# Kernel optimization log

Hardware: AMD Instinct MI355X
Metric: run time of the kernel (lower is better)

## Reference

```python
import jax, jax.numpy as jnp
import numpy as np

E, C, L, B = 8, 128, 1024, 32
FB = L // 2 + 1        # 513 freq bins
HD = 2 * FB            # 1026 hidden dim


def setup_inputs() -> dict:
    key = jax.random.key(0)
    ks = jax.random.split(key, 8)
    return {
        "X_time": jax.random.normal(ks[0], (B, C, L), jnp.float32),
        "bound_params": jax.random.normal(ks[1], (E - 1,), jnp.float32),
        "W1r": jax.random.normal(ks[2], (E, HD, FB), jnp.float32) * 0.1,
        "W1i": jax.random.normal(ks[3], (E, HD, FB), jnp.float32) * 0.1,
        "b1r": jnp.zeros((E, HD), jnp.float32),
        "b1i": jnp.zeros((E, HD), jnp.float32),
        "W2r": jax.random.normal(ks[4], (E, FB, HD), jnp.float32) * 0.1,
        "W2i": jax.random.normal(ks[5], (E, FB, HD), jnp.float32) * 0.1,
        "b2r": jnp.zeros((E, FB), jnp.float32),
        "b2i": jnp.zeros((E, FB), jnp.float32),
        "gate_W": jax.random.normal(ks[6], (E, FB), jnp.float32) * 0.1,
        "gate_b": jnp.zeros((E,), jnp.float32),
    }


def reference(X_time, bound_params, W1r, W1i, b1r, b1i, W2r, W2i, b2r, b2i, gate_W, gate_b):
    Bx, Cx, Lx = X_time.shape
    fb = Lx // 2 + 1
    e = W1r.shape[0]

    Xf = jnp.fft.rfft(X_time, axis=-1)                     # [B,C,FB] complex

    # learnable frequency-band binary masks
    raw = jax.nn.sigmoid(bound_params)
    bounds = jnp.sort(jnp.concatenate([jnp.zeros(1, raw.dtype), raw, jnp.ones(1, raw.dtype)]))
    idx = (bounds * (fb - 1)).astype(jnp.int32)
    starts = idx[:e]
    ends = jnp.concatenate([idx[1:e], jnp.array([fb], jnp.int32)])
    pos = jnp.arange(fb)
    masks = ((pos[None, :] >= starts[:, None]) & (pos[None, :] < ends[:, None])).astype(X_time.dtype)  # [E,FB]

    # masked spectra per expert, split into real/imag: [E,B,C,FB]
    m = masks[:, None, None, :]
    xr = Xf.real * m
    xi = Xf.imag * m

    # expert layer 1: complex linear (W [E,HD,FB]) + complex ReLU
    hr = jnp.einsum('ehf,ebcf->ebch', W1r, xr) - jnp.einsum('ehf,ebcf->ebch', W1i, xi) + b1r[:, None, None, :]
    hi = jnp.einsum('ehf,ebcf->ebch', W1r, xi) + jnp.einsum('ehf,ebcf->ebch', W1i, xr) + b1i[:, None, None, :]
    hr = jax.nn.relu(hr)
    hi = jax.nn.relu(hi)

    # expert layer 2: complex linear (W [E,FB,HD]) -> [E,B,C,FB]
    yr = jnp.einsum('efh,ebch->ebcf', W2r, hr) - jnp.einsum('efh,ebch->ebcf', W2i, hi) + b2r[:, None, None, :]
    yi = jnp.einsum('efh,ebch->ebcf', W2r, hi) + jnp.einsum('efh,ebch->ebcf', W2i, hr) + b2i[:, None, None, :]

    # gate: mean |Xf| over channels -> linear -> softmax over experts
    mag = jnp.mean(jnp.abs(Xf), axis=1)                    # [B,FB]
    gate = jax.nn.softmax(mag @ gate_W.T + gate_b, axis=-1)  # [B,E]

    comb_r = jnp.einsum('ebcf,be->bcf', yr, gate)
    comb_i = jnp.einsum('ebcf,be->bcf', yi, gate)
    return jnp.fft.irfft(jax.lax.complex(comb_r, comb_i), n=Lx, axis=-1)
```

## Files before the change

### kernel.cpp

```cpp
#include <hip/hip_runtime.h>
#include <hip/hip_bf16.h>
#include <math.h>

typedef __hip_bfloat16 bf16;
typedef __attribute__((ext_vector_type(8))) short short8;
typedef __attribute__((ext_vector_type(4))) float f32x4;

#define FB 513
#define HD 1026
#define NN 1024
#define MR 4096
#define NE 8
#define BATCH 32

#define XINT_LD 1280
#define BIAS_LD 1056
#define FINV_LD 1088
#define HP_LD   2080
#define B1_ROWS 2176
#define KCAT    16640
#define MAG_LD  520
#define FF_ROWS 1280

__device__ __forceinline__ void gload16(const void* g, void* l) {
    __builtin_amdgcn_global_load_lds((const __attribute__((address_space(1))) void*)g,
                                     (__attribute__((address_space(3))) void*)l, 16, 0, 0);
}
__device__ __forceinline__ bf16 f2b(float v) { return __float2bfloat16(v); }
__device__ __forceinline__ unsigned short f2bu(float v) {
    bf16 b = __float2bfloat16(v);
    return *reinterpret_cast<unsigned short*>(&b);
}
__device__ __forceinline__ float bu2f(unsigned short u) {
    return __uint_as_float(((unsigned)u) << 16);
}
__device__ __forceinline__ unsigned pack2(float a, float b) {
    return (unsigned)f2bu(a) | ((unsigned)f2bu(b) << 16);
}

__device__ __forceinline__ void xcd_swizzle(int* px, int* py) {
    int gx = gridDim.x;
    int orig = blockIdx.x + gx * blockIdx.y;
    int q = (gx * gridDim.y) >> 3;
    int wg = (orig & 7) * q + (orig >> 3);
    *px = wg % gx;
    *py = wg / gx;
}

__global__ void prep_kernel(const float* __restrict__ bp, int* __restrict__ se) {
    if (threadIdx.x == 0 && blockIdx.x == 0) {
        float b[9];
        b[0] = 0.0f; b[8] = 1.0f;
        for (int i = 0; i < 7; i++) b[i + 1] = 1.0f / (1.0f + expf(-bp[i]));
        for (int i = 1; i < 9; i++) { float v = b[i]; int j = i - 1;
            while (j >= 0 && b[j] > v) { b[j + 1] = b[j]; j--; } b[j + 1] = v; }
        int idx[9];
        for (int i = 0; i < 9; i++) idx[i] = (int)(b[i] * (float)(FB - 1));
        for (int e = 0; e < NE; e++) {
            se[2 * e] = idx[e];
            se[2 * e + 1] = (e < NE - 1) ? idx[e + 1] : FB;
        }
    }
}

#define N_FF  ((long)FF_ROWS * NN)
#define N_FI  (1024L * FINV_LD)
#define N_B1P ((long)NE * B1_ROWS * (XINT_LD / 2))
#define N_XP  ((long)MR * NN / 2)
#define N_PREP (N_FF + N_FI + N_B1P + N_XP)

__global__ void prep_bulk(const float* __restrict__ W1r, const float* __restrict__ W1i,
                          const float* __restrict__ X, const int* __restrict__ se,
                          bf16* __restrict__ Ffwd, bf16* __restrict__ Finv,
                          bf16* __restrict__ B1, bf16* __restrict__ Xb) {
    long i = (long)blockIdx.x * 256 + threadIdx.x;
    const float TWO_PI = 6.283185307179586f;
    if (i < N_FF) {
        int n = (int)(i >> 10), t = (int)(i & (NN - 1));
        float v = 0.0f;
        if (n < 2 * FB) {
            int f = n >> 1, k = (f * t) & (NN - 1);
            float s, c; sincosf(TWO_PI * (float)k / (float)NN, &s, &c);
            v = (n & 1) ? -s : c;
        }
        Ffwd[i] = f2b(v);
        return;
    }
    i -= N_FF;
    if (i < N_FI) {
        int t = (int)(i / FINV_LD), k = (int)(i % FINV_LD);
        float v = 0.0f;
        if (k < 2 * FB) {
            int f = k >> 1, kk = (f * t) & (NN - 1);
            float s, c; sincosf(TWO_PI * (float)kk / (float)NN, &s, &c);
            float cf = (f == 0 || f == FB - 1) ? 1.0f : 2.0f;
            float sc = cf * (1.0f / (float)NN);
            v = (k & 1) ? -s * sc : c * sc;
        }
        Finv[i] = f2b(v);
        return;
    }
    i -= N_FI;
    if (i < N_B1P) {
        int f = (int)(i % (XINT_LD / 2));
        long t = i / (XINT_LD / 2);
        int n = (int)(t % B1_ROWS);
        int e = (int)(t / B1_ROWS);
        float ve = 0.0f, vo = 0.0f;
        if (n < 2 * HD && f < FB && f >= se[2 * e] && f < se[2 * e + 1]) {
            int hi_part = (n >= HD);
            int h = hi_part ? n - HD : n;
            long wi = ((long)e * HD + h) * FB + f;
            float wr = W1r[wi], wim = W1i[wi];
            ve = hi_part ? wim : wr;
            vo = hi_part ? wr : -wim;
        }
        *(unsigned*)(B1 + ((size_t)(e * B1_ROWS + n)) * XINT_LD + 2 * f) = pack2(ve, vo);
        return;
    }
    i -= N_B1P;
    if (i < N_XP) {
        float2 v = ((const float2*)X)[i];
        *(unsigned*)(Xb + 2 * i) = pack2(v.x, v.y);
    }
}

__global__ void pack_B2t(const float* __restrict__ W2r, const float* __restrict__ W2i,
                         bf16* __restrict__ B2t) {
    __shared__ float sR[64][65], sI[64][65];
    int e = blockIdx.z;
    int f0 = blockIdx.x * 64;
    int h0 = blockIdx.y * 64;
    int tid = threadIdx.x;
#pragma unroll
    for (int rep = 0; rep < 16; rep++) {
        int idx = tid + rep * 256;
        int fl = idx >> 6, hl = idx & 63;
        int f = f0 + fl, h = h0 + hl;
        bool ok = (f < FB) && (h < HD);
        size_t wi = ((size_t)e * FB + f) * HD + h;
        sR[fl][hl] = ok ? W2r[wi] : 0.0f;
        sI[fl][hl] = ok ? W2i[wi] : 0.0f;
    }
    __syncthreads();
#pragma unroll
    for (int rep = 0; rep < 4; rep++) {
        int idx = tid + rep * 256;
        int hl = idx >> 4, ch = idx & 15;
        int h = h0 + hl;
        int c0 = 2 * f0 + ch * 8;
        if (c0 >= FINV_LD) continue;
        short8 lo, hi;
#pragma unroll
        for (int j = 0; j < 4; j++) {
            int fl = ch * 4 + j;
            float wr = sR[fl][hl], wim = sI[fl][hl];
            lo[2 * j]     = (short)f2bu(wr);
            lo[2 * j + 1] = (short)f2bu(wim);
            hi[2 * j]     = (short)f2bu(-wim);
            hi[2 * j + 1] = (short)f2bu(wr);
        }
        if (h < HD) {
            *(short8*)(B2t + ((size_t)e * HP_LD + h) * FINV_LD + c0) = lo;
            *(short8*)(B2t + ((size_t)e * HP_LD + HD + h) * FINV_LD + c0) = hi;
        } else if (HD + h < HP_LD) {
            short8 z = {};
            *(short8*)(B2t + ((size_t)e * HP_LD + HD + h) * FINV_LD + c0) = z;
        }
    }
}

__global__ void mag_kernel(const bf16* __restrict__ Xint, float* __restrict__ magp) {
    int b = blockIdx.x, g = blockIdx.y, t = threadIdx.x;
    float acc[3] = {0.0f, 0.0f, 0.0f};
    const bf16* base = Xint + ((size_t)b * 128 + g * 16) * XINT_LD;
    for (int c = 0; c < 16; c++) {
        const bf16* row = base + (size_t)c * XINT_LD;
#pragma unroll
        for (int kk = 0; kk < 3; kk++) {
            int f = t + 256 * kk;
            if (f < FB) {
                float xr = __bfloat162float(row[2 * f]);
                float xi = __bfloat162float(row[2 * f + 1]);
                acc[kk] += sqrtf(xr * xr + xi * xi);
            }
        }
    }
#pragma unroll
    for (int kk = 0; kk < 3; kk++) {
        int f = t + 256 * kk;
        if (f < FB) magp[((size_t)b * 8 + g) * MAG_LD + f] = acc[kk];
    }
}

__global__ void gate_bias_kernel(const float* __restrict__ magp, const float* __restrict__ gW,
                                 const float* __restrict__ gb, const float* __restrict__ b2r,
                                 const float* __restrict__ b2i, float* __restrict__ gate,
                                 float* __restrict__ biasCs) {
    __shared__ float sred[256];
    __shared__ float sg[8];
    int b = blockIdx.x, tid = threadIdx.x;
    int e = tid & 7, j = tid >> 3;
    float acc = 0.0f;
    for (int f = j; f < FB; f += 32) {
        float m = 0.0f;
#pragma unroll
        for (int g = 0; g < 8; g++) m += magp[((size_t)b * 8 + g) * MAG_LD + f];
        acc += m * (1.0f / 128.0f) * gW[e * FB + f];
    }
    sred[tid] = acc;
    __syncthreads();
    if (tid < 64) {
        float a = sred[tid] + sred[tid + 64] + sred[tid + 128] + sred[tid + 192];
        a += __shfl_xor(a, 8); a += __shfl_xor(a, 16); a += __shfl_xor(a, 32);
        float logit = a + gb[e];
        float mx = logit;
        mx = fmaxf(mx, __shfl_xor(mx, 1)); mx = fmaxf(mx, __shfl_xor(mx, 2)); mx = fmaxf(mx, __shfl_xor(mx, 4));
        float ex = expf(logit - mx);
        float sum = ex;
        sum += __shfl_xor(sum, 1); sum += __shfl_xor(sum, 2); sum += __shfl_xor(sum, 4);
        if (tid < 8) { float g_ = ex / sum; sg[tid] = g_; gate[b * NE + tid] = g_; }
    }
    __syncthreads();
    for (int c = tid; c < BIAS_LD; c += 256) {
        float v = 0.0f;
        if (c < 2 * FB) {
            int f = c >> 1;
            const float* bb = (c & 1) ? b2i : b2r;
#pragma unroll
            for (int ee = 0; ee < NE; ee++) v += sg[ee] * bb[ee * FB + f];
            float cf = (f == 0 || f == FB - 1) ? 1.0f : 2.0f;
            v *= cf * (1.0f / (float)NN);
        }
        biasCs[b * BIAS_LD + c] = v;
    }
}

__global__ void biasT_kernel(const float* __restrict__ biasCs, const bf16* __restrict__ Ffwd,
                             float* __restrict__ biasT) {
    int t = blockIdx.x * 256 + threadIdx.x;
    int b = blockIdx.y;
    float s = 0.0f;
    for (int c = 0; c < 2 * FB; c++)
        s += biasCs[b * BIAS_LD + c] * __bfloat162float(Ffwd[(size_t)c * NN + t]);
    biasT[b * NN + t] = s;
}

__global__ void reduce_out4(const bf16* __restrict__ planes, const float* __restrict__ biasT,
                            float* __restrict__ out) {
    long idx = (long)blockIdx.x * 256 + threadIdx.x;
    if (idx >= (long)MR * NN / 8) return;
    size_t base = (size_t)idx * 8;
    long r = base >> 10;
    int t = (int)(base & (NN - 1));
    float s[8] = {};
#pragma unroll
    for (int z = 0; z < 4; z++) {
        short8 v = *(const short8*)(planes + (size_t)z * MR * NN + base);
#pragma unroll
        for (int j = 0; j < 8; j++) s[j] += bu2f((unsigned short)v[j]);
    }
    const float* bT = biasT + (r >> 7) * NN + t;
    float4 o0 = {s[0] + bT[0], s[1] + bT[1], s[2] + bT[2], s[3] + bT[3]};
    float4 o1 = {s[4] + bT[4], s[5] + bT[5], s[6] + bT[6], s[7] + bT[7]};
    *(float4*)(out + base) = o0;
    *(float4*)(out + base + 4) = o1;
}

template <int EPI>
__global__ void gemm_mfma(const bf16* __restrict__ A, int lda,
                          const bf16* __restrict__ B, int ldb, size_t zBstride,
                          void* __restrict__ Cv, int ldc, size_t zCoff,
                          int N, int K, int kPerZ,
                          const int* __restrict__ se2,
                          const float* __restrict__ biasR, const float* __restrict__ biasI,
                          int zBias, const float* __restrict__ gate8) {
    __shared__ bf16 As[128 * 32];
    __shared__ bf16 Bs[128 * 32];
    int tid = threadIdx.x;
    int zz = blockIdx.z;
    int bx, by;
    xcd_swizzle(&bx, &by);
    int row0 = by * 128, col0 = bx * 128;
    const bf16* Bz = B + (size_t)zz * zBstride;

    int kS, kE;
    if (EPI == 1) { int s = se2[2 * zz], e = se2[2 * zz + 1]; kS = (2 * s) & ~31; kE = (2 * e + 31) & ~31; }
    else          { kS = zz * kPerZ; kE = min(K, kS + kPerZ); }

    f32x4 acc[4][4] = {};

    int lane = tid & 63, wid = tid >> 6;
    int wrB = (wid >> 1) << 6, wcB = (wid & 1) << 6;
    int lr = lane & 15, lk = (lane >> 4) << 3;

    int r_a = tid >> 2, c_a = (tid & 3) << 3;
    int r_b = (tid + 256) >> 2, c_b = ((tid + 256) & 3) << 3;

    for (int kt = kS; kt < kE; kt += 32) {
        gload16(A + (size_t)(row0 + r_a) * lda + kt + c_a, &As[(size_t)tid * 8]);
        gload16(A + (size_t)(row0 + r_b) * lda + kt + c_b, &As[((size_t)tid + 256) * 8]);
        gload16(Bz + (size_t)(col0 + r_a) * ldb + kt + c_a, &Bs[(size_t)tid * 8]);
        gload16(Bz + (size_t)(col0 + r_b) * ldb + kt + c_b, &Bs[((size_t)tid + 256) * 8]);
        __syncthreads();
        short8 av[4], bv[4];
#pragma unroll
        for (int m = 0; m < 4; m++)
            av[m] = *(const short8*)&As[(wrB + m * 16 + lr) * 32 + lk];
#pragma unroll
        for (int n = 0; n < 4; n++)
            bv[n] = *(const short8*)&Bs[(wcB + n * 16 + lr) * 32 + lk];
#pragma unroll
        for (int m = 0; m < 4; m++)
#pragma unroll
            for (int n = 0; n < 4; n++)
                acc[m][n] = __builtin_amdgcn_mfma_f32_16x16x32_bf16(av[m], bv[n], acc[m][n], 0, 0, 0);
        __syncthreads();
    }

    int r0 = row0 + wrB + ((lane >> 4) << 2);
    int c0i = col0 + wcB + (lane & 15);
    float g = (EPI == 1) ? gate8[(row0 >> 7) * NE + zz] : 0.0f;

#pragma unroll
    for (int m = 0; m < 4; m++)
#pragma unroll
        for (int n = 0; n < 4; n++) {
            int c = c0i + n * 16;
            if (c >= N) continue;
#pragma unroll
            for (int j = 0; j < 4; j++) {
                int r = r0 + m * 16 + j;
                float v = acc[m][n][j];
                if (EPI == 1) {
                    v += (c < HD) ? biasR[zz * zBias + c] : biasI[zz * zBias + c - HD];
                    v = fmaxf(v, 0.0f) * g;
                    ((bf16*)Cv + (size_t)zz * zCoff)[(size_t)r * ldc + c] = f2b(v);
                } else {
                    ((float*)Cv + (size_t)zz * zCoff)[(size_t)r * ldc + c] = v;
                }
            }
        }
}

__device__ __forceinline__ void stage_half(const bf16* gbase, int ld, int kt,
                                           bf16* ldsBase, int tid) {
#pragma unroll
    for (int j = 0; j < 2; j++) {
        int r = j * 64 + (tid >> 3);
        int sc = ((tid & 7) ^ ((tid >> 3) & 7)) * 8;
        gload16(gbase + (size_t)r * ld + kt + sc, ldsBase + j * 4096 + tid * 8);
    }
}

#define MF(a, b, c) __builtin_amdgcn_mfma_f32_16x16x32_bf16(a, b, c, 0, 0, 0)
#define RD(off) (*(const short8*)(bc + (off)))

#define PHASE_MFMA(FM)                                                        \
    {                                                                         \
        short8 aa0 = RD(aBase + (FM) * 1024 + cb0);                           \
        short8 aa1 = RD(aBase + (FM) * 1024 + cb1);                           \
        short8 ab0 = RD(aBase + (FM + 1) * 1024 + cb0);                       \
        short8 ab1 = RD(aBase + (FM + 1) * 1024 + cb1);                       \
        __builtin_amdgcn_s_setprio(1);                                        \
        acc[FM][0] = MF(aa0, b0[0], acc[FM][0]);                              \
        acc[FM][0] = MF(aa1, b1[0], acc[FM][0]);                              \
        acc[FM][1] = MF(aa0, b0[1], acc[FM][1]);                              \
        acc[FM][1] = MF(aa1, b1[1], acc[FM][1]);                              \
        acc[FM][2] = MF(aa0, b0[2], acc[FM][2]);                              \
        acc[FM][2] = MF(aa1, b1[2], acc[FM][2]);                              \
        acc[FM][3] = MF(aa0, b0[3], acc[FM][3]);                              \
        acc[FM][3] = MF(aa1, b1[3], acc[FM][3]);                              \
        acc[FM + 1][0] = MF(ab0, b0[0], acc[FM + 1][0]);                      \
        acc[FM + 1][0] = MF(ab1, b1[0], acc[FM + 1][0]);                      \
        acc[FM + 1][1] = MF(ab0, b0[1], acc[FM + 1][1]);                      \
        acc[FM + 1][1] = MF(ab1, b1[1], acc[FM + 1][1]);                      \
        acc[FM + 1][2] = MF(ab0, b0[2], acc[FM + 1][2]);                      \
        acc[FM + 1][2] = MF(ab1, b1[2], acc[FM + 1][2]);                      \
        acc[FM + 1][3] = MF(ab0, b0[3], acc[FM + 1][3]);                      \
        acc[FM + 1][3] = MF(ab1, b1[3], acc[FM + 1][3]);                      \
        __builtin_amdgcn_s_setprio(0);                                        \
        __builtin_amdgcn_sched_barrier(0);                                    \
        __builtin_amdgcn_s_barrier();                                         \
    }

template <int SWZ>
__global__ __launch_bounds__(512, 2) void gemm8p(
        const bf16* __restrict__ A, int lda, const bf16* __restrict__ B, int ldb,
        bf16* __restrict__ C, int ldc, size_t zCoff,
        int tilesPerZ, int totTiles, int gx) {
    __shared__ bf16 sm[65536];
    int tid = threadIdx.x;
    int id = blockIdx.x;
    int bx, by, z;
    if (SWZ == 1) {
        int by_z = (id & 7) * 8 + (id >> 5);
        bx = (id >> 3) & 3;
        z = by_z >> 4;
        by = by_z & 15;
    } else {
        bx = id % gx; by = id / gx; z = 0;
    }
    int row0 = by * 256, col0 = bx * 256;
    int t0 = z * tilesPerZ;
    int nt = min(tilesPerZ, totTiles - t0);
    int kS = t0 * 64;

    const bf16* Ab = A + (size_t)row0 * lda;
    const bf16* Bb = B + (size_t)col0 * ldb;

    stage_half(Ab, lda, kS, sm, tid);
    stage_half(Ab + (size_t)128 * lda, lda, kS, sm + 8192, tid);
    stage_half(Bb, ldb, kS, sm + 16384, tid);
    stage_half(Bb + (size_t)128 * ldb, ldb, kS, sm + 24576, tid);

    f32x4 acc[8][4] = {};

    int l = tid & 63, w = tid >> 6;
    int wm = w >> 2, wn = w & 3;
    int lr = l & 15, lk4 = l >> 4;
    int swz = lr & 7;
    int cb0 = ((lk4) ^ swz) * 8;
    int cb1 = ((4 + lk4) ^ swz) * 8;
    int aBaseR = wm * 8192 + lr * 64;
    int bBaseR = 16384 + (wn >> 1) * 8192 + (wn & 1) * 4096 + lr * 64;

    for (int t = 0; t < nt; ++t) {
        const int cur = t & 1;
        const bf16* bc = sm + cur * 32768;
        bf16* bufN = sm + (cur ^ 1) * 32768;
        int aBase = aBaseR, bBase = bBaseR;
        int ktn = kS + (t + 1) * 64;
        bool more = (t + 1) < nt;
        if (more) {
            stage_half(Ab, lda, ktn, bufN, tid);
            stage_half(Ab + (size_t)128 * lda, lda, ktn, bufN + 8192, tid);
            asm volatile("s_waitcnt vmcnt(4)" ::: "memory");
        } else {
            asm volatile("s_waitcnt vmcnt(0)" ::: "memory");
        }
        __builtin_amdgcn_s_barrier();
        __builtin_amdgcn_sched_barrier(0);
        short8 b0[4], b1[4];
#pragma unroll
        for (int n = 0; n < 4; n++) {
            b0[n] = RD(bBase + n * 1024 + cb0);
            b1[n] = RD(bBase + n * 1024 + cb1);
        }
        PHASE_MFMA(0)
        if (more) {
            stage_half(Bb, ldb, ktn, bufN + 16384, tid);
            stage_half(Bb + (size_t)128 * ldb, ldb, ktn, bufN + 24576, tid);
        }
        PHASE_MFMA(2)
        PHASE_MFMA(4)
        PHASE_MFMA(6)
    }

    bf16* Cp = C + (size_t)z * zCoff;
    int rb = row0 + wm * 128 + lk4 * 4;
    int cbase = col0 + wn * 64 + lr;
#pragma unroll
    for (int fm = 0; fm < 8; fm++)
#pragma unroll
        for (int n = 0; n < 4; n++)
#pragma unroll
            for (int j = 0; j < 4; j++)
                Cp[(size_t)(rb + fm * 16 + j) * ldc + cbase + n * 16] = f2b(acc[fm][n][j]);
}

extern "C" void kernel_launch(void* const* d_in, const int* in_sizes, int n_in,
                              void* d_out, int out_size, void* d_ws, size_t ws_size,
                              hipStream_t stream) {
    const float* X   = (const float*)d_in[0];
    const float* bp  = (const float*)d_in[1];
    const float* W1r = (const float*)d_in[2];
    const float* W1i = (const float*)d_in[3];
    const float* b1r = (const float*)d_in[4];
    const float* b1i = (const float*)d_in[5];
    const float* W2r = (const float*)d_in[6];
    const float* W2i = (const float*)d_in[7];
    const float* b2r = (const float*)d_in[8];
    const float* b2i = (const float*)d_in[9];
    const float* gW  = (const float*)d_in[10];
    const float* gb  = (const float*)d_in[11];
    float* out = (float*)d_out;

    const size_t SZH = (size_t)MR * HP_LD * 2;

    char* p = (char*)d_ws;
    auto alloc = [&](size_t bytes) -> char* {
        char* r = p; p += (bytes + 255) & ~255ULL; return r;
    };
    int*   se     = (int*)alloc(64 * 4);
    float* magp   = (float*)alloc((size_t)BATCH * 8 * MAG_LD * 4);
    float* gate   = (float*)alloc((size_t)BATCH * NE * 4);
    float* biasCs = (float*)alloc((size_t)BATCH * BIAS_LD * 4);
    float* biasT  = (float*)alloc((size_t)BATCH * NN * 4);
    bf16*  Ffwd   = (bf16*)alloc((size_t)FF_ROWS * NN * 2);
    bf16*  Finv   = (bf16*)alloc((size_t)NN * FINV_LD * 2);
    bf16*  B1     = (bf16*)alloc((size_t)NE * B1_ROWS * XINT_LD * 2);
    bf16*  B2t    = (bf16*)alloc((size_t)KCAT * FINV_LD * 2);
    bf16*  Xint   = (bf16*)alloc((size_t)MR * XINT_LD * 2);
    bf16*  planesB = (bf16*)alloc(4 * (size_t)MR * NN * 2);
    bf16*  Hp     = (bf16*)alloc(8 * SZH);
    bf16*  B2inv  = (bf16*)B1;
    bf16*  Xb     = (bf16*)((char*)Hp + 8 * SZH - (size_t)MR * NN * 2);

    prep_kernel<<<1, 64, 0, stream>>>(bp, se);
    prep_bulk<<<(unsigned)((N_PREP + 255) / 256), 256, 0, stream>>>(
        W1r, W1i, X, se, Ffwd, Finv, B1, Xb);
    pack_B2t<<<dim3(9, 17, 8), 256, 0, stream>>>(W2r, W2i, B2t);

    gemm8p<0><<<80, 512, 0, stream>>>(
        Xb, NN, Ffwd, NN, Xint, XINT_LD, 0, 16, 16, 5);

    mag_kernel<<<dim3(BATCH, 8), 256, 0, stream>>>(Xint, magp);
    gate_bias_kernel<<<BATCH, 256, 0, stream>>>(magp, gW, gb, b2r, b2i, gate, biasCs);
    biasT_kernel<<<dim3(4, BATCH), 256, 0, stream>>>(biasCs, Ffwd, biasT);

    gemm_mfma<1><<<dim3(17, 32, 8), 256, 0, stream>>>(
        Xint, XINT_LD, B1, XINT_LD, (size_t)B1_ROWS * XINT_LD,
        Hp, KCAT, HP_LD, 2 * HD, 0, 0,
        se, b1r, b1i, HD, gate);

    gemm8p<0><<<260, 512, 0, stream>>>(
        Finv, FINV_LD, B2t, FINV_LD, B2inv, KCAT, 0, 17, 17, 65);

    gemm8p<1><<<256, 512, 0, stream>>>(
        Hp, KCAT, B2inv, KCAT, planesB, NN, (size_t)MR * NN, 65, 260, 4);

    reduce_out4<<<(unsigned)(((size_t)MR * NN / 8 + 255) / 256), 256, 0, stream>>>(
        planesB, biasT, out);
}
```

Baseline: 415.5 us.

## Fold band-bound prep into bulk kernel and prefetch A fragments ahead in gemm8p

```diff
diff --git a/kernel.cpp b/kernel.cpp
--- a/kernel.cpp
+++ b/kernel.cpp
@@ -47,20 +47,13 @@
     *py = wg / gx;
 }
 
-__global__ void prep_kernel(const float* __restrict__ bp, int* __restrict__ se) {
-    if (threadIdx.x == 0 && blockIdx.x == 0) {
-        float b[9];
-        b[0] = 0.0f; b[8] = 1.0f;
-        for (int i = 0; i < 7; i++) b[i + 1] = 1.0f / (1.0f + expf(-bp[i]));
-        for (int i = 1; i < 9; i++) { float v = b[i]; int j = i - 1;
-            while (j >= 0 && b[j] > v) { b[j + 1] = b[j]; j--; } b[j + 1] = v; }
-        int idx[9];
-        for (int i = 0; i < 9; i++) idx[i] = (int)(b[i] * (float)(FB - 1));
-        for (int e = 0; e < NE; e++) {
-            se[2 * e] = idx[e];
-            se[2 * e + 1] = (e < NE - 1) ? idx[e + 1] : FB;
-        }
-    }
+__device__ __forceinline__ void compute_bounds(const float* __restrict__ bp, int* idx) {
+    float b[9];
+    b[0] = 0.0f; b[8] = 1.0f;
+    for (int i = 0; i < 7; i++) b[i + 1] = 1.0f / (1.0f + expf(-bp[i]));
+    for (int i = 1; i < 9; i++) { float v = b[i]; int j = i - 1;
+        while (j >= 0 && b[j] > v) { b[j + 1] = b[j]; j--; } b[j + 1] = v; }
+    for (int i = 0; i < 9; i++) idx[i] = (int)(b[i] * (float)(FB - 1));
 }
 
 #define N_FF  ((long)FF_ROWS * NN)
@@ -70,9 +63,23 @@
 #define N_PREP (N_FF + N_FI + N_B1P + N_XP)
 
 __global__ void prep_bulk(const float* __restrict__ W1r, const float* __restrict__ W1i,
-                          const float* __restrict__ X, const int* __restrict__ se,
+                          const float* __restrict__ X, const float* __restrict__ bp,
+                          int* __restrict__ se,
                           bf16* __restrict__ Ffwd, bf16* __restrict__ Finv,
                           bf16* __restrict__ B1, bf16* __restrict__ Xb) {
+    __shared__ int sse[16];
+    if (threadIdx.x == 0) {
+        int idx[9];
+        compute_bounds(bp, idx);
+        for (int e = 0; e < NE; e++) {
+            sse[2 * e] = idx[e];
+            sse[2 * e + 1] = (e < NE - 1) ? idx[e + 1] : FB;
+        }
+        if (blockIdx.x == 0)
+            for (int k = 0; k < 16; k++) se[k] = sse[k];
+    }
+    __syncthreads();
+
     long i = (long)blockIdx.x * 256 + threadIdx.x;
     const float TWO_PI = 6.283185307179586f;
     if (i < N_FF) {
@@ -107,7 +114,7 @@
         int n = (int)(t % B1_ROWS);
         int e = (int)(t / B1_ROWS);
         float ve = 0.0f, vo = 0.0f;
-        if (n < 2 * HD && f < FB && f >= se[2 * e] && f < se[2 * e + 1]) {
+        if (n < 2 * HD && f < FB && f >= sse[2 * e] && f < sse[2 * e + 1]) {
             int hi_part = (n >= HD);
             int h = hi_part ? n - HD : n;
             long wi = ((long)e * HD + h) * FB + f;
@@ -355,34 +362,31 @@
 
 #define MF(a, b, c) __builtin_amdgcn_mfma_f32_16x16x32_bf16(a, b, c, 0, 0, 0)
 #define RD(off) (*(const short8*)(bc + (off)))
-
-#define PHASE_MFMA(FM)                                                        \
-    {                                                                         \
-        short8 aa0 = RD(aBase + (FM) * 1024 + cb0);                           \
-        short8 aa1 = RD(aBase + (FM) * 1024 + cb1);                           \
-        short8 ab0 = RD(aBase + (FM + 1) * 1024 + cb0);                       \
-        short8 ab1 = RD(aBase + (FM + 1) * 1024 + cb1);                       \
-        __builtin_amdgcn_s_setprio(1);                                        \
-        acc[FM][0] = MF(aa0, b0[0], acc[FM][0]);                              \
-        acc[FM][0] = MF(aa1, b1[0], acc[FM][0]);                              \
-        acc[FM][1] = MF(aa0, b0[1], acc[FM][1]);                              \
-        acc[FM][1] = MF(aa1, b1[1], acc[FM][1]);                              \
-        acc[FM][2] = MF(aa0, b0[2], acc[FM][2]);                              \
-        acc[FM][2] = MF(aa1, b1[2], acc[FM][2]);                              \
-        acc[FM][3] = MF(aa0, b0[3], acc[FM][3]);                              \
-        acc[FM][3] = MF(aa1, b1[3], acc[FM][3]);                              \
-        acc[FM + 1][0] = MF(ab0, b0[0], acc[FM + 1][0]);                      \
-        acc[FM + 1][0] = MF(ab1, b1[0], acc[FM + 1][0]);                      \
-        acc[FM + 1][1] = MF(ab0, b0[1], acc[FM + 1][1]);                      \
-        acc[FM + 1][1] = MF(ab1, b1[1], acc[FM + 1][1]);                      \
-        acc[FM + 1][2] = MF(ab0, b0[2], acc[FM + 1][2]);                      \
-        acc[FM + 1][2] = MF(ab1, b1[2], acc[FM + 1][2]);                      \
-        acc[FM + 1][3] = MF(ab0, b0[3], acc[FM + 1][3]);                      \
-        acc[FM + 1][3] = MF(ab1, b1[3], acc[FM + 1][3]);                      \
-        __builtin_amdgcn_s_setprio(0);                                        \
-        __builtin_amdgcn_sched_barrier(0);                                    \
-        __builtin_amdgcn_s_barrier();                                         \
-    }
+#define LOADA(dst, FM)                                                        \
+    dst[0] = RD(aBase + (FM) * 1024 + cb0);                                   \
+    dst[1] = RD(aBase + (FM) * 1024 + cb1);                                   \
+    dst[2] = RD(aBase + (FM + 1) * 1024 + cb0);                               \
+    dst[3] = RD(aBase + (FM + 1) * 1024 + cb1);
+#define CLUST(FM, av)                                                         \
+    __builtin_amdgcn_s_setprio(1);                                            \
+    acc[FM][0] = MF(av[0], b0[0], acc[FM][0]);                                \
+    acc[FM][0] = MF(av[1], b1[0], acc[FM][0]);                                \
+    acc[FM][1] = MF(av[0], b0[1], acc[FM][1]);                                \
+    acc[FM][1] = MF(av[1], b1[1], acc[FM][1]);                                \
+    acc[FM][2] = MF(av[0], b0[2], acc[FM][2]);                                \
+    acc[FM][2] = MF(av[1], b1[2], acc[FM][2]);                                \
+    acc[FM][3] = MF(av[0], b0[3], acc[FM][3]);                                \
+    acc[FM][3] = MF(av[1], b1[3], acc[FM][3]);                                \
+    acc[FM + 1][0] = MF(av[2], b0[0], acc[FM + 1][0]);                        \
+    acc[FM + 1][0] = MF(av[3], b1[0], acc[FM + 1][0]);                        \
+    acc[FM + 1][1] = MF(av[2], b0[1], acc[FM + 1][1]);                        \
+    acc[FM + 1][1] = MF(av[3], b1[1], acc[FM + 1][1]);                        \
+    acc[FM + 1][2] = MF(av[2], b0[2], acc[FM + 1][2]);                        \
+    acc[FM + 1][2] = MF(av[3], b1[2], acc[FM + 1][2]);                        \
+    acc[FM + 1][3] = MF(av[2], b0[3], acc[FM + 1][3]);                        \
+    acc[FM + 1][3] = MF(av[3], b1[3], acc[FM + 1][3]);                        \
+    __builtin_amdgcn_s_setprio(0);
+#define PBAR { __builtin_amdgcn_sched_barrier(0); __builtin_amdgcn_s_barrier(); }
 
 template <int SWZ>
 __global__ __launch_bounds__(512, 2) void gemm8p(
@@ -422,14 +426,13 @@
     int swz = lr & 7;
     int cb0 = ((lk4) ^ swz) * 8;
     int cb1 = ((4 + lk4) ^ swz) * 8;
-    int aBaseR = wm * 8192 + lr * 64;
-    int bBaseR = 16384 + (wn >> 1) * 8192 + (wn & 1) * 4096 + lr * 64;
+    int aBase = wm * 8192 + lr * 64;
+    int bBase = 16384 + (wn >> 1) * 8192 + (wn & 1) * 4096 + lr * 64;
 
     for (int t = 0; t < nt; ++t) {
         const int cur = t & 1;
         const bf16* bc = sm + cur * 32768;
         bf16* bufN = sm + (cur ^ 1) * 32768;
-        int aBase = aBaseR, bBase = bBaseR;
         int ktn = kS + (t + 1) * 64;
         bool more = (t + 1) < nt;
         if (more) {
@@ -441,20 +444,29 @@
         }
         __builtin_amdgcn_s_barrier();
         __builtin_amdgcn_sched_barrier(0);
-        short8 b0[4], b1[4];
+        short8 b0[4], b1[4], a0[4], a1[4], a2[4], a3[4];
 #pragma unroll
         for (int n = 0; n < 4; n++) {
             b0[n] = RD(bBase + n * 1024 + cb0);
             b1[n] = RD(bBase + n * 1024 + cb1);
         }
-        PHASE_MFMA(0)
+        LOADA(a0, 0)
+        LOADA(a1, 2)
+        __builtin_amdgcn_sched_barrier(0);
+        CLUST(0, a0)
         if (more) {
             stage_half(Bb, ldb, ktn, bufN + 16384, tid);
             stage_half(Bb + (size_t)128 * ldb, ldb, ktn, bufN + 24576, tid);
         }
-        PHASE_MFMA(2)
-        PHASE_MFMA(4)
-        PHASE_MFMA(6)
+        LOADA(a2, 4)
+        PBAR
+        CLUST(2, a1)
+        LOADA(a3, 6)
+        PBAR
+        CLUST(4, a2)
+        PBAR
+        CLUST(6, a3)
+        PBAR
     }
 
     bf16* Cp = C + (size_t)z * zCoff;
@@ -507,9 +519,8 @@
     bf16*  B2inv  = (bf16*)B1;
     bf16*  Xb     = (bf16*)((char*)Hp + 8 * SZH - (size_t)MR * NN * 2);
 
-    prep_kernel<<<1, 64, 0, stream>>>(bp, se);
     prep_bulk<<<(unsigned)((N_PREP + 255) / 256), 256, 0, stream>>>(
-        W1r, W1i, X, se, Ffwd, Finv, B1, Xb);
+        W1r, W1i, X, bp, se, Ffwd, Finv, B1, Xb);
     pack_B2t<<<dim3(9, 17, 8), 256, 0, stream>>>(W2r, W2i, B2t);
 
     gemm8p<0><<<80, 512, 0, stream>>>(
```

Measured after the change: 423.7 us. About the same (+2.0%).
